# Performance work log

Hardware: AMD Instinct MI355X
Metric: run time of the kernel (lower is better)

## Reference

```python
import jax, jax.numpy as jnp
import numpy as np

B, H, S, D = 4, 16, 1024, 64
MAX_REL = 16  # max_relative_position


def setup_inputs() -> dict:
    key = jax.random.key(0)
    kq, kk, kv, kr = jax.random.split(key, 4)
    Q = jax.random.normal(kq, (B, H, S, D), dtype=jnp.float32)
    K = jax.random.normal(kk, (B, H, S, D), dtype=jnp.float32)
    V = jax.random.normal(kv, (B, H, S, D), dtype=jnp.float32)
    # learned relative-position embedding table [2*P+1, d_k]
    rel_table = jax.random.normal(kr, (2 * MAX_REL + 1, D), dtype=jnp.float32) * 0.02
    # causal mask, broadcastable over batch/heads; 0 => masked
    mask = jnp.tril(jnp.ones((S, S), dtype=jnp.int32))[None, None, :, :]
    return {"Q": Q, "K": K, "V": V, "rel_table": rel_table, "mask": mask}


def reference(Q, K, V, rel_table, mask):
    scale = jnp.sqrt(jnp.asarray(Q.shape[-1], Q.dtype))
    seq_len = Q.shape[2]
    r = jnp.arange(seq_len)
    # clipped relative distances -> embedding indices in [0, 2P]
    idx = jnp.clip(r[None, :] - r[:, None], -MAX_REL, MAX_REL) + MAX_REL  # [S,S]
    rel_emb = rel_table[idx]  # [S, S, D]
    scores = jnp.einsum('bhld,bhrd->bhlr', Q, K) / scale  # [B,H,S,S]
    scores = scores + jnp.einsum('bhld,lrd->bhlr', Q, rel_emb)
    scores = jnp.where(mask == 0, -jnp.inf, scores)
    attn = jax.nn.softmax(scores, axis=-1)
    output = jnp.einsum('bhlr,bhrd->bhld', attn, V)  # [B,H,S,D]
    return (output, attn)
```

## Files before the change

kernel.cpp:

```cpp
#include <hip/hip_runtime.h>

#define S_ 1024
#define D_ 64
#define RT 32
#define SCP 1036

typedef _Float16 f16x4 __attribute__((ext_vector_type(4)));
typedef _Float16 f16x8 __attribute__((ext_vector_type(8)));
typedef __fp16  h16x2 __attribute__((ext_vector_type(2)));
typedef float f32x4 __attribute__((ext_vector_type(4)));

__global__ __launch_bounds__(256)
void prep_k(const float* __restrict__ K, _Float16* __restrict__ Kws) {
    const int idx = blockIdx.x * 256 + threadIdx.x;
    const int bh  = idx >> 12;
    const int kt  = (idx >> 6) & 63;
    const int l15 = (idx >> 2) & 15;
    const int g4  = idx & 3;
    const float* kp = K + ((size_t)bh * S_ + kt * 16 + l15) * D_ + 4 * g4;
    _Float16* dst = Kws + ((size_t)(bh * 64 + kt) * 16 + l15) * 64 + g4 * 16;
    f16x8 o0, o1;
    #pragma unroll
    for (int h = 0; h < 4; ++h) {
        float4 f = *reinterpret_cast<const float4*>(kp + 16 * h);
        h16x2 lo = __builtin_amdgcn_cvt_pkrtz(f.x, f.y);
        h16x2 hi = __builtin_amdgcn_cvt_pkrtz(f.z, f.w);
        if (h < 2) {
            o0[4*h+0] = (_Float16)lo[0]; o0[4*h+1] = (_Float16)lo[1];
            o0[4*h+2] = (_Float16)hi[0]; o0[4*h+3] = (_Float16)hi[1];
        } else {
            o1[4*(h-2)+0] = (_Float16)lo[0]; o1[4*(h-2)+1] = (_Float16)lo[1];
            o1[4*(h-2)+2] = (_Float16)hi[0]; o1[4*(h-2)+3] = (_Float16)hi[1];
        }
    }
    *reinterpret_cast<f16x8*>(dst)     = o0;
    *reinterpret_cast<f16x8*>(dst + 8) = o1;
}

__global__ __launch_bounds__(256)
void prep_v(const float* __restrict__ V, _Float16* __restrict__ VT) {
    const int idx = blockIdx.x * 256 + threadIdx.x;
    const int bh  = idx >> 12;
    const int kt  = (idx >> 6) & 63;
    const int col = idx & 63;
    const float* vp = V + ((size_t)bh * S_ + kt * 16) * D_ + col;
    _Float16* dst = VT + ((size_t)(bh * 64 + kt) * 64 + col) * 16;
    f16x8 a, b;
    #pragma unroll
    for (int kk = 0; kk < 16; ++kk) {
        float f = vp[(size_t)kk * D_];
        if (kk < 8) a[kk] = (_Float16)f; else b[kk - 8] = (_Float16)f;
    }
    *reinterpret_cast<f16x8*>(dst)     = a;
    *reinterpret_cast<f16x8*>(dst + 8) = b;
}

__global__ __launch_bounds__(512, 4)
void relattn_main(const float* __restrict__ Q, const float* __restrict__ rel,
                  const _Float16* __restrict__ Kws, const _Float16* __restrict__ VT,
                  float* __restrict__ outO, float* outA) {
    __shared__ __align__(16) _Float16 sc[RT * SCP];
    __shared__ float qrel[RT * 17];
    __shared__ float rowsum[4][RT];

    const int tid  = threadIdx.x;
    const int lane = tid & 63;
    const int w    = tid >> 6;
    const int rh   = w >> 2;
    const int cg   = w & 3;
    const int l15  = lane & 15;
    const int g4   = lane >> 4;
    const int bid  = blockIdx.x;
    const int bh   = (bid & 7) + 8 * (bid >> 8);
    const int tile = 31 - ((bid >> 3) & 31);
    const int R0   = tile * RT;
    const int nt16 = 2 * tile + 2;
    const int lrow = 16 * rh + l15;

    const float* Qb = Q + (size_t)bh * S_ * D_;
    const _Float16* Kb = Kws + (size_t)bh * 64 * 1024;
    const _Float16* Vt = VT  + (size_t)bh * 64 * 1024;

    {
        const int z0 = 16 * nt16;
        const f16x8 zz = {0, 0, 0, 0, 0, 0, 0, 0};
        const int i = tid >> 4;
        for (int c = z0 + (tid & 15) * 8; c < S_; c += 128)
            *reinterpret_cast<f16x8*>(&sc[i * SCP + c]) = zz;
    }

    {
        int idx = tid;
        #pragma unroll
        for (int rep = 0; rep < 2; ++rep) {
            if (idx < RT * 17) {
                const int i = idx / 17;
                const int j = idx - i * 17;
                const float* qp = Qb + (size_t)(R0 + i) * D_;
                const float* rp = rel + j * D_;
                float s = 0.f;
                #pragma unroll
                for (int d = 0; d < D_; d += 4) {
                    float4 a = *reinterpret_cast<const float4*>(qp + d);
                    float4 b = *reinterpret_cast<const float4*>(rp + d);
                    s += a.x * b.x + a.y * b.y + a.z * b.z + a.w * b.w;
                }
                qrel[idx] = s;
            }
            idx = 512 + tid;
        }
    }

    f16x4 aq[4];
    {
        const float* qp = Qb + (size_t)(R0 + lrow) * D_ + 4 * g4;
        #pragma unroll
        for (int h = 0; h < 4; ++h) {
            float4 f = *reinterpret_cast<const float4*>(qp + 16 * h);
            aq[h] = f16x4{(_Float16)(f.x * 0.125f), (_Float16)(f.y * 0.125f),
                          (_Float16)(f.z * 0.125f), (_Float16)(f.w * 0.125f)};
        }
    }

    __syncthreads();

    const int   myrow = R0 + lrow;
    const float qr0v  = qrel[lrow * 17];
    const int fastmax = (R0 + 16 * rh - 31) >> 4;

    float psum = 0.f;
    auto qk_load = [&](int ct, f16x8* kf) {
        const _Float16* kp = Kb + ((size_t)ct * 16 + l15) * 64 + g4 * 16;
        kf[0] = *reinterpret_cast<const f16x8*>(kp);
        kf[1] = *reinterpret_cast<const f16x8*>(kp + 8);
    };
    auto qk_compute = [&](int ct, const f16x8* kf) {
        f32x4 acc = {0.f, 0.f, 0.f, 0.f};
        __builtin_amdgcn_s_setprio(1);
        #pragma unroll
        for (int h = 0; h < 4; ++h) {
            f16x4 ka = {kf[h >> 1][(h & 1) * 4 + 0], kf[h >> 1][(h & 1) * 4 + 1],
                        kf[h >> 1][(h & 1) * 4 + 2], kf[h >> 1][(h & 1) * 4 + 3]};
            acc = __builtin_amdgcn_mfma_f32_16x16x16f16(ka, aq[h], acc, 0, 0, 0);
        }
        __builtin_amdgcn_s_setprio(0);
        float e[4];
        if (ct <= fastmax) {
            #pragma unroll
            for (int j = 0; j < 4; ++j) e[j] = __expf(acc[j] + qr0v);
        } else {
            #pragma unroll
            for (int j = 0; j < 4; ++j) {
                const int dlt = myrow - (ct * 16 + 4 * g4 + j);
                e[j] = 0.f;
                if (dlt >= 0)
                    e[j] = __expf(acc[j] + ((dlt < 16) ? qrel[lrow * 17 + 16 - dlt]
                                                       : qr0v));
            }
        }
        psum += (e[0] + e[1]) + (e[2] + e[3]);
        h16x2 lo = __builtin_amdgcn_cvt_pkrtz(e[0], e[1]);
        h16x2 hi = __builtin_amdgcn_cvt_pkrtz(e[2], e[3]);
        f16x4 pk = {(_Float16)lo[0], (_Float16)lo[1],
                    (_Float16)hi[0], (_Float16)hi[1]};
        *reinterpret_cast<f16x4*>(&sc[lrow * SCP + ct * 16 + 4 * g4]) = pk;
    };

    for (int ct0 = cg; ct0 < nt16; ct0 += 16) {
        f16x8 k0[2], k1[2], k2[2], k3[2];
        const bool h1 = (ct0 + 4)  < nt16;
        const bool h2 = (ct0 + 8)  < nt16;
        const bool h3 = (ct0 + 12) < nt16;
        qk_load(ct0, k0);
        if (h1) qk_load(ct0 + 4,  k1);
        if (h2) qk_load(ct0 + 8,  k2);
        if (h3) qk_load(ct0 + 12, k3);
        qk_compute(ct0, k0);
        if (h1) qk_compute(ct0 + 4,  k1);
        if (h2) qk_compute(ct0 + 8,  k2);
        if (h3) qk_compute(ct0 + 12, k3);
    }

    psum += __shfl_xor(psum, 16);
    psum += __shfl_xor(psum, 32);
    if (lane < 16) rowsum[cg][16 * rh + lane] = psum;
    __syncthreads();

    const int n0    = 16 * cg;
    const int ktile = 2 * tile + rh + 1;
    const int fg    = ktile >> 2;
    const int tail  = ktile & 3;
    const _Float16* vtb = Vt + ((size_t)(n0 + l15)) * 16 + 4 * g4;

    f16x4 bvA[4], bvB[4], bvC[4];
    auto pv_load = [&](int g, f16x4* bv) {
        #pragma unroll
        for (int u = 0; u < 4; ++u)
            bv[u] = *reinterpret_cast<const f16x4*>(vtb + (size_t)(4 * g + u) * 1024);
    };
    f32x4 oa[4] = {{0,0,0,0},{0,0,0,0},{0,0,0,0},{0,0,0,0}};
    auto pv_mfma = [&](int g, const f16x4* bv) {
        __builtin_amdgcn_s_setprio(1);
        #pragma unroll
        for (int u = 0; u < 4; ++u) {
            f16x4 ap = *reinterpret_cast<f16x4*>(
                &sc[lrow * SCP + (4 * g + u) * 16 + 4 * g4]);
            oa[u] = __builtin_amdgcn_mfma_f32_16x16x16f16(ap, bv[u], oa[u], 0, 0, 0);
        }
        __builtin_amdgcn_s_setprio(0);
    };

    if (fg > 0) pv_load(0, bvA);
    if (fg > 1) pv_load(1, bvB);

    float* Ab = outA + ((size_t)bh * S_ + R0) * S_;
    #pragma unroll
    for (int ii = 0; ii < 4; ++ii) {
        const int i = 4 * w + ii;
        const float iv = 1.f / (rowsum[0][i] + rowsum[1][i] +
                                rowsum[2][i] + rowsum[3][i]);
        #pragma unroll
        for (int q = 0; q < 4; ++q) {
            const int c = q * 256 + lane * 4;
            f16x4 sv = *reinterpret_cast<f16x4*>(&sc[i * SCP + c]);
            f32x4 o = {(float)sv[0] * iv, (float)sv[1] * iv,
                       (float)sv[2] * iv, (float)sv[3] * iv};
            __builtin_nontemporal_store(
                o, reinterpret_cast<f32x4*>(Ab + (size_t)i * S_ + c));
        }
    }

    if (fg > 2) pv_load(2, bvC);
    int g = 0;
    for (; g + 3 < fg; g += 3) {
        pv_mfma(g, bvA);
        pv_load(g + 3, bvA);
        pv_mfma(g + 1, bvB);
        if (g + 4 < fg) pv_load(g + 4, bvB);
        pv_mfma(g + 2, bvC);
        if (g + 5 < fg) pv_load(g + 5, bvC);
    }
    if (g < fg)     pv_mfma(g, bvA);
    if (g + 1 < fg) pv_mfma(g + 1, bvB);
    if (g + 2 < fg) pv_mfma(g + 2, bvC);

    for (int r = 0; r < tail; ++r) {
        const int kt = 4 * fg + r;
        f16x4 bv = *reinterpret_cast<const f16x4*>(vtb + (size_t)kt * 1024);
        f16x4 ap = *reinterpret_cast<f16x4*>(&sc[lrow * SCP + kt * 16 + 4 * g4]);
        oa[r] = __builtin_amdgcn_mfma_f32_16x16x16f16(ap, bv, oa[r], 0, 0, 0);
    }

    f32x4 op = (oa[0] + oa[1]) + (oa[2] + oa[3]);

    float* Ob = outO + (size_t)bh * S_ * D_;
    #pragma unroll
    for (int j = 0; j < 4; ++j) {
        const int row = 16 * rh + 4 * g4 + j;
        const float s = rowsum[0][row] + rowsum[1][row] +
                        rowsum[2][row] + rowsum[3][row];
        Ob[(size_t)(R0 + row) * D_ + n0 + l15] = op[j] / s;
    }
}

extern "C" void kernel_launch(void* const* d_in, const int* in_sizes, int n_in,
                              void* d_out, int out_size, void* d_ws, size_t ws_size,
                              hipStream_t stream) {
    const float* Q   = (const float*)d_in[0];
    const float* K   = (const float*)d_in[1];
    const float* V   = (const float*)d_in[2];
    const float* rel = (const float*)d_in[3];

    float* out  = (float*)d_out;
    float* outO = out;
    float* outA = out + (size_t)4 * 16 * 1024 * 64;

    _Float16*  Kws  = (_Float16*)((char*)d_ws + (size_t)(1 << 20));
    _Float16*  VTws = (_Float16*)((char*)d_ws + (size_t)(10 << 20));

    prep_k<<<dim3(1024), dim3(256), 0, stream>>>(K, Kws);
    prep_v<<<dim3(1024), dim3(256), 0, stream>>>(V, VTws);
    relattn_main<<<dim3(2048), dim3(512), 0, stream>>>(Q, rel, Kws, VTws,
                                                       outO, outA);
}
```

Baseline: 133.1 us.

## Halve row tile to 16 with 256-thread blocks and use 16x16x32 MFMA

Each block now owns 16 query rows with 4 waves instead of 32 rows with 8 waves, and the grid doubles to 4096 blocks. The K workspace becomes plain row-major fp16, so QK^T runs as two 16x16x32 f16 MFMAs per tile instead of four 16x16x16 ones. The first V-fragment prefetch is moved ahead of the row-sum barrier so its latency overlaps the reduction. The aim is finer causal load balancing, more blocks in flight and fewer MFMA issues. The cost is that each K/V tile is re-read by twice as many blocks, and per-block setup such as the qrel dot products is repeated more often.

After: 125.1 us. 1.06x faster.

```diff
diff --git a/kernel.cpp b/kernel.cpp
--- a/kernel.cpp
+++ b/kernel.cpp
@@ -2,7 +2,7 @@
 
 #define S_ 1024
 #define D_ 64
-#define RT 32
+#define RT 16
 #define SCP 1036
 
 typedef _Float16 f16x4 __attribute__((ext_vector_type(4)));
@@ -13,25 +13,19 @@
 __global__ __launch_bounds__(256)
 void prep_k(const float* __restrict__ K, _Float16* __restrict__ Kws) {
     const int idx = blockIdx.x * 256 + threadIdx.x;
-    const int bh  = idx >> 12;
-    const int kt  = (idx >> 6) & 63;
-    const int l15 = (idx >> 2) & 15;
     const int g4  = idx & 3;
-    const float* kp = K + ((size_t)bh * S_ + kt * 16 + l15) * D_ + 4 * g4;
-    _Float16* dst = Kws + ((size_t)(bh * 64 + kt) * 16 + l15) * 64 + g4 * 16;
+    const float* kp = K + (size_t)(idx >> 2) * 64 + g4 * 16;
+    _Float16* dst = Kws + (size_t)(idx >> 2) * 64 + g4 * 16;
     f16x8 o0, o1;
     #pragma unroll
-    for (int h = 0; h < 4; ++h) {
-        float4 f = *reinterpret_cast<const float4*>(kp + 16 * h);
-        h16x2 lo = __builtin_amdgcn_cvt_pkrtz(f.x, f.y);
-        h16x2 hi = __builtin_amdgcn_cvt_pkrtz(f.z, f.w);
-        if (h < 2) {
-            o0[4*h+0] = (_Float16)lo[0]; o0[4*h+1] = (_Float16)lo[1];
-            o0[4*h+2] = (_Float16)hi[0]; o0[4*h+3] = (_Float16)hi[1];
-        } else {
-            o1[4*(h-2)+0] = (_Float16)lo[0]; o1[4*(h-2)+1] = (_Float16)lo[1];
-            o1[4*(h-2)+2] = (_Float16)hi[0]; o1[4*(h-2)+3] = (_Float16)hi[1];
-        }
+    for (int u = 0; u < 2; ++u) {
+        float4 f0 = *reinterpret_cast<const float4*>(kp + 8 * u);
+        float4 f1 = *reinterpret_cast<const float4*>(kp + 8 * u + 4);
+        f16x8& o = u ? o1 : o0;
+        o[0] = (_Float16)f0.x; o[1] = (_Float16)f0.y;
+        o[2] = (_Float16)f0.z; o[3] = (_Float16)f0.w;
+        o[4] = (_Float16)f1.x; o[5] = (_Float16)f1.y;
+        o[6] = (_Float16)f1.z; o[7] = (_Float16)f1.w;
     }
     *reinterpret_cast<f16x8*>(dst)     = o0;
     *reinterpret_cast<f16x8*>(dst + 8) = o1;
@@ -55,7 +49,7 @@
     *reinterpret_cast<f16x8*>(dst + 8) = b;
 }
 
-__global__ __launch_bounds__(512, 4)
+__global__ __launch_bounds__(256, 4)
 void relattn_main(const float* __restrict__ Q, const float* __restrict__ rel,
                   const _Float16* __restrict__ Kws, const _Float16* __restrict__ VT,
                   float* __restrict__ outO, float* outA) {
@@ -66,16 +60,13 @@
     const int tid  = threadIdx.x;
     const int lane = tid & 63;
     const int w    = tid >> 6;
-    const int rh   = w >> 2;
-    const int cg   = w & 3;
     const int l15  = lane & 15;
     const int g4   = lane >> 4;
     const int bid  = blockIdx.x;
-    const int bh   = (bid & 7) + 8 * (bid >> 8);
-    const int tile = 31 - ((bid >> 3) & 31);
+    const int bh   = (bid & 7) + 8 * (bid >> 9);
+    const int tile = 63 - ((bid >> 3) & 63);
     const int R0   = tile * RT;
-    const int nt16 = 2 * tile + 2;
-    const int lrow = 16 * rh + l15;
+    const int nt16 = tile + 1;
 
     const float* Qb = Q + (size_t)bh * S_ * D_;
     const _Float16* Kb = Kws + (size_t)bh * 64 * 1024;
@@ -107,42 +98,44 @@
                 }
                 qrel[idx] = s;
             }
-            idx = 512 + tid;
-        }
-    }
-
-    f16x4 aq[4];
+            idx = 256 + tid;
+        }
+    }
+
+    f16x8 aq0, aq1;
     {
-        const float* qp = Qb + (size_t)(R0 + lrow) * D_ + 4 * g4;
-        #pragma unroll
-        for (int h = 0; h < 4; ++h) {
-            float4 f = *reinterpret_cast<const float4*>(qp + 16 * h);
-            aq[h] = f16x4{(_Float16)(f.x * 0.125f), (_Float16)(f.y * 0.125f),
-                          (_Float16)(f.z * 0.125f), (_Float16)(f.w * 0.125f)};
-        }
+        const float* qp = Qb + (size_t)(R0 + l15) * D_ + 8 * g4;
+        float4 f0 = *reinterpret_cast<const float4*>(qp);
+        float4 f1 = *reinterpret_cast<const float4*>(qp + 4);
+        float4 f2 = *reinterpret_cast<const float4*>(qp + 32);
+        float4 f3 = *reinterpret_cast<const float4*>(qp + 36);
+        aq0 = f16x8{(_Float16)(f0.x*0.125f), (_Float16)(f0.y*0.125f),
+                    (_Float16)(f0.z*0.125f), (_Float16)(f0.w*0.125f),
+                    (_Float16)(f1.x*0.125f), (_Float16)(f1.y*0.125f),
+                    (_Float16)(f1.z*0.125f), (_Float16)(f1.w*0.125f)};
+        aq1 = f16x8{(_Float16)(f2.x*0.125f), (_Float16)(f2.y*0.125f),
+                    (_Float16)(f2.z*0.125f), (_Float16)(f2.w*0.125f),
+                    (_Float16)(f3.x*0.125f), (_Float16)(f3.y*0.125f),
+                    (_Float16)(f3.z*0.125f), (_Float16)(f3.w*0.125f)};
     }
 
     __syncthreads();
 
-    const int   myrow = R0 + lrow;
-    const float qr0v  = qrel[lrow * 17];
-    const int fastmax = (R0 + 16 * rh - 31) >> 4;
+    const int   myrow = R0 + l15;
+    const float qr0v  = qrel[l15 * 17];
+    const int fastmax = (R0 - 31) >> 4;
 
     float psum = 0.f;
     auto qk_load = [&](int ct, f16x8* kf) {
-        const _Float16* kp = Kb + ((size_t)ct * 16 + l15) * 64 + g4 * 16;
+        const _Float16* kp = Kb + ((size_t)ct * 16 + l15) * 64 + 8 * g4;
         kf[0] = *reinterpret_cast<const f16x8*>(kp);
-        kf[1] = *reinterpret_cast<const f16x8*>(kp + 8);
+        kf[1] = *reinterpret_cast<const f16x8*>(kp + 32);
     };
     auto qk_compute = [&](int ct, const f16x8* kf) {
         f32x4 acc = {0.f, 0.f, 0.f, 0.f};
         __builtin_amdgcn_s_setprio(1);
-        #pragma unroll
-        for (int h = 0; h < 4; ++h) {
-            f16x4 ka = {kf[h >> 1][(h & 1) * 4 + 0], kf[h >> 1][(h & 1) * 4 + 1],
-                        kf[h >> 1][(h & 1) * 4 + 2], kf[h >> 1][(h & 1) * 4 + 3]};
-            acc = __builtin_amdgcn_mfma_f32_16x16x16f16(ka, aq[h], acc, 0, 0, 0);
-        }
+        acc = __builtin_amdgcn_mfma_f32_16x16x32_f16(kf[0], aq0, acc, 0, 0, 0);
+        acc = __builtin_amdgcn_mfma_f32_16x16x32_f16(kf[1], aq1, acc, 0, 0, 0);
         __builtin_amdgcn_s_setprio(0);
         float e[4];
         if (ct <= fastmax) {
@@ -154,7 +147,7 @@
                 const int dlt = myrow - (ct * 16 + 4 * g4 + j);
                 e[j] = 0.f;
                 if (dlt >= 0)
-                    e[j] = __expf(acc[j] + ((dlt < 16) ? qrel[lrow * 17 + 16 - dlt]
+                    e[j] = __expf(acc[j] + ((dlt < 16) ? qrel[l15 * 17 + 16 - dlt]
                                                        : qr0v));
             }
         }
@@ -163,10 +156,10 @@
         h16x2 hi = __builtin_amdgcn_cvt_pkrtz(e[2], e[3]);
         f16x4 pk = {(_Float16)lo[0], (_Float16)lo[1],
                     (_Float16)hi[0], (_Float16)hi[1]};
-        *reinterpret_cast<f16x4*>(&sc[lrow * SCP + ct * 16 + 4 * g4]) = pk;
-    };
-
-    for (int ct0 = cg; ct0 < nt16; ct0 += 16) {
+        *reinterpret_cast<f16x4*>(&sc[l15 * SCP + ct * 16 + 4 * g4]) = pk;
+    };
+
+    for (int ct0 = w; ct0 < nt16; ct0 += 16) {
         f16x8 k0[2], k1[2], k2[2], k3[2];
         const bool h1 = (ct0 + 4)  < nt16;
         const bool h2 = (ct0 + 8)  < nt16;
@@ -181,13 +174,8 @@
         if (h3) qk_compute(ct0 + 12, k3);
     }
 
-    psum += __shfl_xor(psum, 16);
-    psum += __shfl_xor(psum, 32);
-    if (lane < 16) rowsum[cg][16 * rh + lane] = psum;
-    __syncthreads();
-
-    const int n0    = 16 * cg;
-    const int ktile = 2 * tile + rh + 1;
+    const int n0    = 16 * w;
+    const int ktile = nt16;
     const int fg    = ktile >> 2;
     const int tail  = ktile & 3;
     const _Float16* vtb = Vt + ((size_t)(n0 + l15)) * 16 + 4 * g4;
@@ -198,20 +186,25 @@
         for (int u = 0; u < 4; ++u)
             bv[u] = *reinterpret_cast<const f16x4*>(vtb + (size_t)(4 * g + u) * 1024);
     };
+    if (fg > 0) pv_load(0, bvA);
+    if (fg > 1) pv_load(1, bvB);
+
+    psum += __shfl_xor(psum, 16);
+    psum += __shfl_xor(psum, 32);
+    if (lane < 16) rowsum[w][lane] = psum;
+    __syncthreads();
+
     f32x4 oa[4] = {{0,0,0,0},{0,0,0,0},{0,0,0,0},{0,0,0,0}};
     auto pv_mfma = [&](int g, const f16x4* bv) {
         __builtin_amdgcn_s_setprio(1);
         #pragma unroll
         for (int u = 0; u < 4; ++u) {
             f16x4 ap = *reinterpret_cast<f16x4*>(
-                &sc[lrow * SCP + (4 * g + u) * 16 + 4 * g4]);
+                &sc[l15 * SCP + (4 * g + u) * 16 + 4 * g4]);
             oa[u] = __builtin_amdgcn_mfma_f32_16x16x16f16(ap, bv[u], oa[u], 0, 0, 0);
         }
         __builtin_amdgcn_s_setprio(0);
     };
-
-    if (fg > 0) pv_load(0, bvA);
-    if (fg > 1) pv_load(1, bvB);
 
     float* Ab = outA + ((size_t)bh * S_ + R0) * S_;
     #pragma unroll
@@ -247,7 +240,7 @@
     for (int r = 0; r < tail; ++r) {
         const int kt = 4 * fg + r;
         f16x4 bv = *reinterpret_cast<const f16x4*>(vtb + (size_t)kt * 1024);
-        f16x4 ap = *reinterpret_cast<f16x4*>(&sc[lrow * SCP + kt * 16 + 4 * g4]);
+        f16x4 ap = *reinterpret_cast<f16x4*>(&sc[l15 * SCP + kt * 16 + 4 * g4]);
         oa[r] = __builtin_amdgcn_mfma_f32_16x16x16f16(ap, bv, oa[r], 0, 0, 0);
     }
 
@@ -256,7 +249,7 @@
     float* Ob = outO + (size_t)bh * S_ * D_;
     #pragma unroll
     for (int j = 0; j < 4; ++j) {
-        const int row = 16 * rh + 4 * g4 + j;
+        const int row = 4 * g4 + j;
         const float s = rowsum[0][row] + rowsum[1][row] +
                         rowsum[2][row] + rowsum[3][row];
         Ob[(size_t)(R0 + row) * D_ + n0 + l15] = op[j] / s;
@@ -280,6 +273,6 @@
 
     prep_k<<<dim3(1024), dim3(256), 0, stream>>>(K, Kws);
     prep_v<<<dim3(1024), dim3(256), 0, stream>>>(V, VTws);
-    relattn_main<<<dim3(2048), dim3(512), 0, stream>>>(Q, rel, Kws, VTws,
+    relattn_main<<<dim3(4096), dim3(256), 0, stream>>>(Q, rel, Kws, VTws,
                                                        outO, outA);
 }
```
